# Performance work log

Measured on AMD Instinct MI355X. Metric: run time of the kernel, lower is better.

## Reference

```python
import jax, jax.numpy as jnp
import numpy as np

B, S, D, H = 4, 2048, 1024, 16
HD = D // H  # head_dim = 64


def setup_inputs() -> dict:
    key = jax.random.key(0)
    k1, k2, k3, k4, k5 = jax.random.split(key, 5)
    x = jax.random.normal(k1, (B, S, D), dtype=jnp.float32)
    # per-head QKV projection weights (H separate Linear(D, 3*HD) layers, batched)
    Wqkv = jax.random.normal(k2, (H, D, 3 * HD), dtype=jnp.float32) * (D ** -0.5)
    bqkv = jax.random.normal(k3, (H, 3 * HD), dtype=jnp.float32) * 0.02
    # output projection Linear(D, D)
    Wo = jax.random.normal(k4, (D, D), dtype=jnp.float32) * (D ** -0.5)
    bo = jax.random.normal(k5, (D,), dtype=jnp.float32) * 0.02
    return {"x": x, "Wqkv": Wqkv, "bqkv": bqkv, "Wo": Wo, "bo": bo}


def reference(x, Wqkv, bqkv, Wo, bo):
    # Batched per-head QKV projection: [B,S,D] x [H,D,3*HD] -> [B,H,S,3*HD]
    qkv = jnp.einsum('bsd,hde->bhse', x, Wqkv) + bqkv[None, :, None, :]
    q, k, v = jnp.split(qkv, 3, axis=-1)  # each [B,H,S,HD]
    scale = HD ** -0.5
    scores = jnp.einsum('bhqe,bhke->bhqk', q, k) * scale  # [B,H,S,S]
    causal = jnp.tril(jnp.ones((S, S), dtype=bool))
    scores = jnp.where(causal, scores, -jnp.inf)
    attn = jax.nn.softmax(scores, axis=-1)
    # dropout is identity in eval mode
    out = jnp.einsum('bhqk,bhke->bhqe', attn, v)  # [B,H,S,HD]
    out = jnp.transpose(out, (0, 2, 1, 3)).reshape(B, S, D)  # concat heads
    return out @ Wo + bo
```

## Files before the change

### kernel.cpp

```cpp
#include <hip/hip_runtime.h>
#include <hip/hip_bf16.h>

#define B_ 4
#define S_ 2048
#define D_ 1024
#define H_ 16
#define HD_ 64
#define M_TOK 8192
#define QSCALE 0.18033688f

typedef __attribute__((ext_vector_type(4))) float f32x4;
typedef __attribute__((ext_vector_type(8))) short short8;
typedef __attribute__((ext_vector_type(4))) short short4_t;

__device__ inline short f2bf(float f) {
  unsigned u = __builtin_bit_cast(unsigned, f);
  u += 0x7fff + ((u >> 16) & 1);
  return (short)(u >> 16);
}
__device__ inline short f2bf_trunc(float f) {
  return (short)(__builtin_bit_cast(unsigned, f) >> 16);
}

typedef __attribute__((address_space(1))) const unsigned int gas_u32;
typedef __attribute__((address_space(3))) unsigned int las_u32;
__device__ inline void gload_lds16(const void* g, void* l) {
  __builtin_amdgcn_global_load_lds((gas_u32*)g, (las_u32*)l, 16, 0, 0);
}


__global__ __launch_bounds__(256) void conv_x_kernel(
    const float* __restrict__ x, short* __restrict__ xb) {
  size_t base = ((size_t)blockIdx.x * 256 + threadIdx.x) * 8;
  f32x4 v0 = *reinterpret_cast<const f32x4*>(&x[base]);
  f32x4 v1 = *reinterpret_cast<const f32x4*>(&x[base + 4]);
  short8 o;
  o[0]=f2bf(v0[0]); o[1]=f2bf(v0[1]); o[2]=f2bf(v0[2]); o[3]=f2bf(v0[3]);
  o[4]=f2bf(v1[0]); o[5]=f2bf(v1[1]); o[6]=f2bf(v1[2]); o[7]=f2bf(v1[3]);
  *reinterpret_cast<short8*>(&xb[base]) = o;
}

__global__ __launch_bounds__(256) void conv_wqkv_kernel(
    const float* __restrict__ Wqkv, short* __restrict__ wp) {
  const int h = blockIdx.x;
  const int k0 = blockIdx.y * 32;
  const int tid = threadIdx.x;
  __shared__ short T[192 * 40];
#pragma unroll
  for (int i = 0; i < 6; ++i) {
    int iv = tid + i * 256;
    int k = iv / 48;
    int e4 = (iv % 48) * 4;
    f32x4 v = *reinterpret_cast<const f32x4*>(&Wqkv[((size_t)h * D_ + k0 + k) * 192 + e4]);
#pragma unroll
    for (int j = 0; j < 4; ++j) T[(e4 + j) * 40 + k] = f2bf(v[j]);
  }
  __syncthreads();
#pragma unroll
  for (int i = 0; i < 3; ++i) {
    int u = tid + i * 256;
    int e16 = u >> 6;
    int rem = u & 63;
    int e = e16 * 16 + (rem & 15);
    int k8 = (rem >> 4) * 8;
    short8 o = *reinterpret_cast<const short8*>(&T[e * 40 + k8]);
    *reinterpret_cast<short8*>(
        &wp[(size_t)(h * 12 + e16) * 16384 + blockIdx.y * 512 + rem * 8]) = o;
  }
}

__global__ __launch_bounds__(256) void conv_wo_kernel(
    const float* __restrict__ Wo, short* __restrict__ wp) {
  const int k0 = blockIdx.x * 32;
  const int n0 = blockIdx.y * 128;
  const int tid = threadIdx.x;
  __shared__ short T[128 * 40];
#pragma unroll
  for (int i = 0; i < 4; ++i) {
    int iv = tid + i * 256;
    int k = iv >> 5;
    int n4 = (iv & 31) * 4;
    f32x4 v = *reinterpret_cast<const f32x4*>(&Wo[(size_t)(k0 + k) * 1024 + n0 + n4]);
#pragma unroll
    for (int j = 0; j < 4; ++j) T[(n4 + j) * 40 + k] = f2bf(v[j]);
  }
  __syncthreads();
#pragma unroll
  for (int i = 0; i < 2; ++i) {
    int u = tid + i * 256;
    int ntile = u >> 6;
    int rem = u & 63;
    short8 o = *reinterpret_cast<const short8*>(
        &T[(ntile * 16 + (rem & 15)) * 40 + (rem >> 4) * 8]);
    *reinterpret_cast<short8*>(
        &wp[(size_t)((n0 >> 4) + ntile) * 16384 + blockIdx.x * 512 + rem * 8]) = o;
  }
}

template<int EPI>
__global__ __launch_bounds__(256, 3) void gemm4_kernel(
    const short* __restrict__ A, const short* __restrict__ Bp,
    const float* __restrict__ bias,
    short* __restrict__ qb, short* __restrict__ kb, short* __restrict__ vt,
    float* __restrict__ out) {
  constexpr int KD = 1024;
  constexpr int NKT = KD / 32;
  const int m0 = blockIdx.x * 128;
  const int n0 = blockIdx.y * 128;
  const int tid = threadIdx.x;
  const int lane = tid & 63, wv = tid >> 6;
  const int wr = wv >> 1, wc = wv & 1;
  const int g = lane >> 4, c = lane & 15;

  __shared__ short As[4 * 4096];

  const f32x4 zero4 = {0.f, 0.f, 0.f, 0.f};
  f32x4 acc[4][4];
#pragma unroll
  for (int i = 0; i < 4; ++i)
#pragma unroll
    for (int j = 0; j < 4; ++j) acc[i][j] = zero4;

  const short* bbase = Bp + (size_t)((n0 + wc * 64) >> 4) * 16384 + lane * 8;
  short8 bb0[4], bb1[4];

  auto LOADB = [&](int t, short8* br) {
#pragma unroll
    for (int nt = 0; nt < 4; ++nt)
      br[nt] = *reinterpret_cast<const short8*>(&bbase[(size_t)nt * 16384 + t * 512]);
  };
  auto STAGE = [&](int kt, int buf) {
    const short* asrc = A + (size_t)m0 * KD + kt * 32;
#pragma unroll
    for (int i = 0; i < 2; ++i) {
      int ch = tid + i * 256;
      int row = ch >> 2;
      int slot = (ch & 3) ^ ((row >> 1) & 3);
      gload_lds16(asrc + (size_t)row * KD + slot * 8, &As[buf * 4096 + ch * 8]);
    }
  };
  const int sread = (g ^ ((c >> 1) & 3)) * 8;
  auto COMP = [&](int buf, short8* br) {
    const short* Ab = &As[buf * 4096];
    short8 a[4];
#pragma unroll
    for (int mt = 0; mt < 4; ++mt)
      a[mt] = *reinterpret_cast<const short8*>(&Ab[(wr * 64 + mt * 16 + c) * 32 + sread]);
    __builtin_amdgcn_s_setprio(1);
#pragma unroll
    for (int mt = 0; mt < 4; ++mt)
#pragma unroll
      for (int nt = 0; nt < 4; ++nt)
        acc[mt][nt] = __builtin_amdgcn_mfma_f32_16x16x32_bf16(a[mt], br[nt], acc[mt][nt], 0, 0, 0);
    __builtin_amdgcn_s_setprio(0);
  };

#define BAR1 __builtin_amdgcn_sched_barrier(0); __builtin_amdgcn_s_barrier(); __builtin_amdgcn_sched_barrier(0)
#define VMW(N) asm volatile("s_waitcnt vmcnt(" #N ")" ::: "memory")

  STAGE(0, 0); STAGE(1, 1); LOADB(0, bb0);

#pragma unroll 1
  for (int p = 0; p < 7; ++p) {
    const int tb = p * 4;
    BAR1; STAGE(tb + 2, 2); LOADB(tb + 1, bb1); VMW(6); BAR1; COMP(0, bb0);
    BAR1; STAGE(tb + 3, 3); LOADB(tb + 2, bb0); VMW(6); BAR1; COMP(1, bb1);
    BAR1; STAGE(tb + 4, 0); LOADB(tb + 3, bb1); VMW(6); BAR1; COMP(2, bb0);
    BAR1; STAGE(tb + 5, 1); LOADB(tb + 4, bb0); VMW(6); BAR1; COMP(3, bb1);
  }
  BAR1; STAGE(30, 2); LOADB(29, bb1); VMW(6); BAR1; COMP(0, bb0);
  BAR1; STAGE(31, 3); LOADB(30, bb0); VMW(6); BAR1; COMP(1, bb1);
  BAR1;               LOADB(31, bb1); VMW(4); BAR1; COMP(2, bb0);
  BAR1;                               VMW(0); BAR1; COMP(3, bb1);

#undef BAR1
#undef VMW

#pragma unroll
  for (int mt = 0; mt < 4; ++mt) {
#pragma unroll
    for (int nt = 0; nt < 4; ++nt) {
      int n = n0 + wc * 64 + nt * 16 + c;
      float bv = bias[n];
      int m_base = m0 + wr * 64 + mt * 16 + g * 4;
      if (EPI == 0) {
        int h = n / 192, e = n % 192;
        int bb2 = m_base >> 11, s0 = m_base & 2047;
        size_t plane = (size_t)(bb2 * H_ + h) * (S_ * HD_);
        if (e < 64) {
          size_t bp = plane + (size_t)(s0 >> 4) * 1024 + (e >> 3) * 128 + (s0 & 15) * 8 + (e & 7);
#pragma unroll
          for (int r = 0; r < 4; ++r)
            qb[bp + r * 8] = f2bf((acc[mt][nt][r] + bv) * QSCALE);
        } else if (e < 128) {
          int ek = e - 64;
          size_t bp = plane + (size_t)(s0 >> 4) * 1024 + (ek >> 3) * 128 + (s0 & 15) * 8 + (ek & 7);
#pragma unroll
          for (int r = 0; r < 4; ++r)
            kb[bp + r * 8] = f2bf(acc[mt][nt][r] + bv);
        } else {
          int hd = e - 128;
          size_t bp = plane + (size_t)((hd >> 4) * 64 + (s0 >> 5)) * 512 +
                      ((s0 >> 3) & 3) * 128 + (hd & 15) * 8 + (s0 & 7);
          short4_t vv;
#pragma unroll
          for (int r = 0; r < 4; ++r) vv[r] = f2bf(acc[mt][nt][r] + bv);
          *reinterpret_cast<short4_t*>(&vt[bp]) = vv;
        }
      } else {
#pragma unroll
        for (int r = 0; r < 4; ++r)
          out[(size_t)(m_base + r) * D_ + n] = acc[mt][nt][r] + bv;
      }
    }
  }
}

struct KF32 { short8 f[4]; };

__device__ __forceinline__ void load_kf32(KF32& k, const short* __restrict__ kbh,
                                          int ktb, int lane) {
#pragma unroll
  for (int cc = 0; cc < 2; ++cc)
#pragma unroll
    for (int t = 0; t < 2; ++t)
      k.f[cc * 2 + t] = *reinterpret_cast<const short8*>(
          &kbh[(size_t)(ktb * 2 + t) * 1024 + cc * 512 + lane * 8]);
}

__global__ __launch_bounds__(256, 4) void attn_kernel(
    const short* __restrict__ qb, const short* __restrict__ kb,
    const short* __restrict__ vt, short* __restrict__ av) {
  const int orig = blockIdx.x;
  const int xcd = orig & 7;
  const int local = orig >> 3;
  const int bh = xcd * 8 + (local & 7);
  const int qt = 15 - (local >> 3);
  const int bb = bh >> 4, h = bh & 15;
  const int tid = threadIdx.x;
  const int lane = tid & 63, wv = tid >> 6;
  const int g = lane >> 4, c = lane & 15;
  const int q0 = qt * 128;
  const int r0 = q0 + wv * 32;

  __shared__ short Ps[4][32 * 40];
  short* Pw = Ps[wv];

  const short* qbh = qb + (size_t)bh * S_ * HD_;
  const short* kbh = kb + (size_t)bh * S_ * HD_;
  const short* vth = vt + (size_t)bh * HD_ * S_;

  short8 ones;
#pragma unroll
  for (int j = 0; j < 8; ++j) ones[j] = (short)0x3F80;

  const f32x4 zero4 = {0.f, 0.f, 0.f, 0.f};

  short8 qf[2][2];
#pragma unroll
  for (int mt = 0; mt < 2; ++mt)
#pragma unroll
    for (int cc = 0; cc < 2; ++cc)
      qf[mt][cc] = *reinterpret_cast<const short8*>(
          &qbh[(size_t)(r0 / 16 + mt) * 1024 + cc * 512 + lane * 8]);

  f32x4 acc_o[2][4];
  f32x4 lacc[2];
#pragma unroll
  for (int mt = 0; mt < 2; ++mt) {
    lacc[mt] = zero4;
#pragma unroll
    for (int nt = 0; nt < 4; ++nt) acc_o[mt][nt] = zero4;
  }

  const int diag = 4 * qt + wv;
  const int nk = diag + 1;

  KF32 kA, kB;
  load_kf32(kA, kbh, 0, lane);

  auto body = [&](int ktb, KF32& kc, KF32& kn) {
    const int k0 = ktb * 32;
    short8 vf[4];
#pragma unroll
    for (int nt = 0; nt < 4; ++nt)
      vf[nt] = *reinterpret_cast<const short8*>(
          &vth[(size_t)(nt * 64 + ktb) * 512 + lane * 8]);
    f32x4 sc[2][2];
#pragma unroll
    for (int mt = 0; mt < 2; ++mt)
#pragma unroll
      for (int t = 0; t < 2; ++t) sc[mt][t] = zero4;
#pragma unroll
    for (int cc = 0; cc < 2; ++cc)
#pragma unroll
      for (int mt = 0; mt < 2; ++mt)
#pragma unroll
        for (int t = 0; t < 2; ++t)
          sc[mt][t] = __builtin_amdgcn_mfma_f32_16x16x32_bf16(
              qf[mt][cc], kc.f[cc * 2 + t], sc[mt][t], 0, 0, 0);
    int ktbn = ktb + 1;
    if (ktbn >= S_ / 32) ktbn = 0;
    load_kf32(kn, kbh, ktbn, lane);
    if (ktb == diag) {
#pragma unroll
      for (int mt = 0; mt < 2; ++mt)
#pragma unroll
        for (int t = 0; t < 2; ++t) {
          const int key = k0 + t * 16 + c;
#pragma unroll
          for (int r = 0; r < 4; ++r) {
            const int qi = r0 + mt * 16 + g * 4 + r;
            if (key > qi) sc[mt][t][r] = -INFINITY;
          }
        }
    }
#pragma unroll
    for (int mt = 0; mt < 2; ++mt)
#pragma unroll
      for (int t = 0; t < 2; ++t)
#pragma unroll
        for (int r = 0; r < 4; ++r) {
          float pf = __builtin_exp2f(sc[mt][t][r]);
          Pw[(mt * 16 + g * 4 + r) * 40 + t * 16 + c] = f2bf_trunc(pf);
        }
    short8 pa[2];
#pragma unroll
    for (int mt = 0; mt < 2; ++mt)
      pa[mt] = *reinterpret_cast<const short8*>(&Pw[(mt * 16 + c) * 40 + g * 8]);
#pragma unroll
    for (int mt = 0; mt < 2; ++mt)
      lacc[mt] = __builtin_amdgcn_mfma_f32_16x16x32_bf16(pa[mt], ones, lacc[mt], 0, 0, 0);
#pragma unroll
    for (int mt = 0; mt < 2; ++mt)
#pragma unroll
      for (int nt = 0; nt < 4; ++nt)
        acc_o[mt][nt] = __builtin_amdgcn_mfma_f32_16x16x32_bf16(
            pa[mt], vf[nt], acc_o[mt][nt], 0, 0, 0);
  };

  int ktb = 0;
  for (; ktb + 1 < nk; ktb += 2) {
    body(ktb,     kA, kB);
    body(ktb + 1, kB, kA);
  }
  if (ktb < nk) body(ktb, kA, kB);

#pragma unroll
  for (int mt = 0; mt < 2; ++mt) {
    float inv[4];
#pragma unroll
    for (int r = 0; r < 4; ++r) inv[r] = 1.0f / lacc[mt][r];
#pragma unroll
    for (int nt = 0; nt < 4; ++nt)
#pragma unroll
      for (int r = 0; r < 4; ++r) {
        int R = r0 + mt * 16 + g * 4 + r;
        av[(size_t)(bb * S_ + R) * D_ + h * HD_ + nt * 16 + c] =
            f2bf(acc_o[mt][nt][r] * inv[r]);
      }
  }
}

extern "C" void kernel_launch(void* const* d_in, const int* in_sizes, int n_in,
                              void* d_out, int out_size, void* d_ws, size_t ws_size,
                              hipStream_t stream) {
  const float* x    = (const float*)d_in[0];
  const float* Wqkv = (const float*)d_in[1];
  const float* bqkv = (const float*)d_in[2];
  const float* Wo   = (const float*)d_in[3];
  const float* bo   = (const float*)d_in[4];
  float* out = (float*)d_out;

  const size_t NTOK = (size_t)B_ * H_ * S_ * HD_;
  short* xb    = (short*)d_ws;
  short* wqkvt = xb + (size_t)M_TOK * D_;
  short* wot   = wqkvt + (size_t)3072 * 1024;
  short* qb    = wot + (size_t)1024 * 1024;
  short* kb    = qb + NTOK;
  short* vt    = kb + NTOK;
  short* av    = xb;

  conv_x_kernel   <<<4096, 256, 0, stream>>>(x, xb);
  conv_wqkv_kernel<<<dim3(16, 32), 256, 0, stream>>>(Wqkv, wqkvt);
  conv_wo_kernel  <<<dim3(32, 8), 256, 0, stream>>>(Wo, wot);
  gemm4_kernel<0> <<<dim3(64, 24), 256, 0, stream>>>(xb, wqkvt, bqkv, qb, kb, vt, nullptr);
  attn_kernel     <<<1024, 256, 0, stream>>>(qb, kb, vt, av);
  gemm4_kernel<1> <<<dim3(64, 8), 256, 0, stream>>>(av, wot, bo, nullptr, nullptr, nullptr, out);
}
```

Baseline: 165.9 us.

## Pack bf16 pairs in V and P stores, interleave q-tile order, lower attn occupancy

The QKV epilogue now writes V^T as packed bf16 pairs from two adjacent m-tiles using a 128-bit store, which changes the V^T interleave layout to pair keys across tiles. The attention P tile is also written as packed 32-bit words via byte-permute truncation, halving the LDS store count. Block-to-work mapping now interleaves long and short causal q-tiles within each XCD to balance load, and the attention launch bound drops from 4 to 3 blocks per SIMD to free registers. This relies on the attention kernel's V fragment reads and the P-tile key ordering being consistent with the new packed layouts. V is now rounded by truncation where it was previously round-to-nearest.

```diff
diff --git a/kernel.cpp b/kernel.cpp
--- a/kernel.cpp
+++ b/kernel.cpp
@@ -10,6 +10,7 @@
 #define QSCALE 0.18033688f
 
 typedef __attribute__((ext_vector_type(4))) float f32x4;
+typedef __attribute__((ext_vector_type(4))) int int4_t;
 typedef __attribute__((ext_vector_type(8))) short short8;
 typedef __attribute__((ext_vector_type(4))) short short4_t;
 
@@ -20,6 +21,10 @@
 }
 __device__ inline short f2bf_trunc(float f) {
   return (short)(__builtin_bit_cast(unsigned, f) >> 16);
+}
+__device__ inline unsigned pack_bf16_trunc(float lo, float hi) {
+  return __builtin_amdgcn_perm(__builtin_bit_cast(unsigned, hi),
+                               __builtin_bit_cast(unsigned, lo), 0x07060302u);
 }
 
 typedef __attribute__((address_space(1))) const unsigned int gas_u32;
@@ -104,7 +109,6 @@
     short* __restrict__ qb, short* __restrict__ kb, short* __restrict__ vt,
     float* __restrict__ out) {
   constexpr int KD = 1024;
-  constexpr int NKT = KD / 32;
   const int m0 = blockIdx.x * 128;
   const int n0 = blockIdx.y * 128;
   const int tid = threadIdx.x;
@@ -176,38 +180,57 @@
 #undef BAR1
 #undef VMW
 
-#pragma unroll
-  for (int mt = 0; mt < 4; ++mt) {
+  if (EPI == 0) {
 #pragma unroll
     for (int nt = 0; nt < 4; ++nt) {
       int n = n0 + wc * 64 + nt * 16 + c;
       float bv = bias[n];
-      int m_base = m0 + wr * 64 + mt * 16 + g * 4;
-      if (EPI == 0) {
-        int h = n / 192, e = n % 192;
-        int bb2 = m_base >> 11, s0 = m_base & 2047;
-        size_t plane = (size_t)(bb2 * H_ + h) * (S_ * HD_);
-        if (e < 64) {
-          size_t bp = plane + (size_t)(s0 >> 4) * 1024 + (e >> 3) * 128 + (s0 & 15) * 8 + (e & 7);
-#pragma unroll
-          for (int r = 0; r < 4; ++r)
-            qb[bp + r * 8] = f2bf((acc[mt][nt][r] + bv) * QSCALE);
-        } else if (e < 128) {
-          int ek = e - 64;
-          size_t bp = plane + (size_t)(s0 >> 4) * 1024 + (ek >> 3) * 128 + (s0 & 15) * 8 + (ek & 7);
-#pragma unroll
-          for (int r = 0; r < 4; ++r)
-            kb[bp + r * 8] = f2bf(acc[mt][nt][r] + bv);
-        } else {
-          int hd = e - 128;
-          size_t bp = plane + (size_t)((hd >> 4) * 64 + (s0 >> 5)) * 512 +
-                      ((s0 >> 3) & 3) * 128 + (hd & 15) * 8 + (s0 & 7);
-          short4_t vv;
-#pragma unroll
-          for (int r = 0; r < 4; ++r) vv[r] = f2bf(acc[mt][nt][r] + bv);
-          *reinterpret_cast<short4_t*>(&vt[bp]) = vv;
+      int h = n / 192, e = n % 192;
+      if (e < 128) {
+#pragma unroll
+        for (int mt = 0; mt < 4; ++mt) {
+          int m_base = m0 + wr * 64 + mt * 16 + g * 4;
+          int bb2 = m_base >> 11, s0 = m_base & 2047;
+          size_t plane = (size_t)(bb2 * H_ + h) * (S_ * HD_);
+          if (e < 64) {
+            size_t bp = plane + (size_t)(s0 >> 4) * 1024 + (e >> 3) * 128 + (s0 & 15) * 8 + (e & 7);
+#pragma unroll
+            for (int r = 0; r < 4; ++r)
+              qb[bp + r * 8] = f2bf((acc[mt][nt][r] + bv) * QSCALE);
+          } else {
+            int ek = e - 64;
+            size_t bp = plane + (size_t)(s0 >> 4) * 1024 + (ek >> 3) * 128 + (s0 & 15) * 8 + (ek & 7);
+#pragma unroll
+            for (int r = 0; r < 4; ++r)
+              kb[bp + r * 8] = f2bf(acc[mt][nt][r] + bv);
+          }
         }
       } else {
+        int hd = e - 128;
+#pragma unroll
+        for (int mtp = 0; mtp < 2; ++mtp) {
+          int mt = mtp * 2;
+          int m_base = m0 + wr * 64 + mt * 16 + g * 4;
+          int bb2 = m_base >> 11, s0 = m_base & 2047;
+          size_t plane = (size_t)(bb2 * H_ + h) * (S_ * HD_);
+          size_t bp = plane + (size_t)((hd >> 4) * 64 + (s0 >> 5)) * 512 +
+                      ((s0 >> 2) & 3) * 128 + (hd & 15) * 8;
+          int4_t pk;
+#pragma unroll
+          for (int r = 0; r < 4; ++r)
+            pk[r] = (int)pack_bf16_trunc(acc[mt][nt][r] + bv, acc[mt + 1][nt][r] + bv);
+          *reinterpret_cast<int4_t*>(&vt[bp]) = pk;
+        }
+      }
+    }
+  } else {
+#pragma unroll
+    for (int mt = 0; mt < 4; ++mt) {
+#pragma unroll
+      for (int nt = 0; nt < 4; ++nt) {
+        int n = n0 + wc * 64 + nt * 16 + c;
+        float bv = bias[n];
+        int m_base = m0 + wr * 64 + mt * 16 + g * 4;
 #pragma unroll
         for (int r = 0; r < 4; ++r)
           out[(size_t)(m_base + r) * D_ + n] = acc[mt][nt][r] + bv;
@@ -228,14 +251,15 @@
           &kbh[(size_t)(ktb * 2 + t) * 1024 + cc * 512 + lane * 8]);
 }
 
-__global__ __launch_bounds__(256, 4) void attn_kernel(
+__global__ __launch_bounds__(256, 3) void attn_kernel(
     const short* __restrict__ qb, const short* __restrict__ kb,
     const short* __restrict__ vt, short* __restrict__ av) {
   const int orig = blockIdx.x;
   const int xcd = orig & 7;
   const int local = orig >> 3;
-  const int bh = xcd * 8 + (local & 7);
-  const int qt = 15 - (local >> 3);
+  const int bh = xcd * 8 + (local >> 4);
+  const int qi = local & 15;
+  const int qt = (qi & 1) ? (qi >> 1) : 15 - (qi >> 1);
   const int bb = bh >> 4, h = bh & 15;
   const int tid = threadIdx.x;
   const int lane = tid & 63, wv = tid >> 6;
@@ -245,6 +269,7 @@
 
   __shared__ short Ps[4][32 * 40];
   short* Pw = Ps[wv];
+  unsigned* Pw32 = reinterpret_cast<unsigned*>(Pw);
 
   const short* qbh = qb + (size_t)bh * S_ * HD_;
   const short* kbh = kb + (size_t)bh * S_ * HD_;
@@ -310,20 +335,19 @@
           const int key = k0 + t * 16 + c;
 #pragma unroll
           for (int r = 0; r < 4; ++r) {
-            const int qi = r0 + mt * 16 + g * 4 + r;
-            if (key > qi) sc[mt][t][r] = -INFINITY;
+            const int qi2 = r0 + mt * 16 + g * 4 + r;
+            if (key > qi2) sc[mt][t][r] = -INFINITY;
           }
         }
     }
 #pragma unroll
     for (int mt = 0; mt < 2; ++mt)
 #pragma unroll
-      for (int t = 0; t < 2; ++t)
-#pragma unroll
-        for (int r = 0; r < 4; ++r) {
-          float pf = __builtin_exp2f(sc[mt][t][r]);
-          Pw[(mt * 16 + g * 4 + r) * 40 + t * 16 + c] = f2bf_trunc(pf);
-        }
+      for (int r = 0; r < 4; ++r) {
+        float p0 = __builtin_exp2f(sc[mt][0][r]);
+        float p1 = __builtin_exp2f(sc[mt][1][r]);
+        Pw32[(mt * 16 + g * 4 + r) * 20 + c] = pack_bf16_trunc(p0, p1);
+      }
     short8 pa[2];
 #pragma unroll
     for (int mt = 0; mt < 2; ++mt)
```

After: 197.6 us. +19.1%, slower.
